# Kernel optimization log

Hardware: AMD Instinct MI355X
Metric: run time of the kernel (lower is better)

The kernel has to match this reference:

```python
import jax, jax.numpy as jnp
import numpy as np

NUM_HEADS = 8
LN_EPS = 1e-5


def setup_inputs() -> dict:
    key = jax.random.key(0)
    ks = jax.random.split(key, 8)
    B, H, W, C = 2, 64, 64, 256
    return {
        "x": jax.random.normal(ks[0], (B, H, W, C), dtype=jnp.float32),
        "cond": jax.random.normal(ks[1], (B, C), dtype=jnp.float32),
        "t": jax.random.randint(ks[2], (B,), 0, 100, dtype=jnp.int64),
        "emb_table": jax.random.normal(ks[3], (100, C), dtype=jnp.float32) * 0.02,
        "ada_w": jax.random.normal(ks[4], (C, 2 * C), dtype=jnp.float32) * 0.02,
        "ada_b": jnp.zeros((2 * C,), dtype=jnp.float32),
        "qkv_w": jax.random.normal(ks[5], (C, 3 * C), dtype=jnp.float32) * 0.02,
        "qkv_b": jnp.zeros((3 * C,), dtype=jnp.float32),
        "proj_w": jax.random.normal(ks[6], (C, C), dtype=jnp.float32) * 0.02,
        "proj_b": jnp.zeros((C,), dtype=jnp.float32),
    }


def reference(x, cond, t, emb_table, ada_w, ada_b, qkv_w, qkv_b, proj_w, proj_b):
    B, H, W, C = x.shape
    N = H * W
    h = NUM_HEADS
    d = C // h
    scale = d ** -0.5

    x = x.reshape(B, N, C)

    # AdaLayerNorm (adalayernorm_abs): timestep embedding -> SiLU -> Linear -> scale/shift
    emb = emb_table[t]                                # [B, C]
    ss = jax.nn.silu(emb) @ ada_w + ada_b             # [B, 2C]
    sc, sh = jnp.split(ss, 2, axis=-1)                # each [B, C]
    mu = jnp.mean(x, axis=-1, keepdims=True)
    var = jnp.var(x, axis=-1, keepdims=True)
    xn = (x - mu) * jax.lax.rsqrt(var + LN_EPS)       # LN without affine
    x = xn * (1.0 + sc[:, None, :]) + sh[:, None, :]

    # QKV projection and head split
    qkv = (x @ qkv_w + qkv_b).reshape(B, N, 3, h, d)
    qkv = jnp.transpose(qkv, (2, 0, 3, 1, 4))          # [3, B, h, N, d]
    q, k, v = qkv[0], qkv[1], qkv[2]

    # Manual attention: full [B, h, N, N] scores (matches original module)
    attn = jnp.einsum('bhnd,bhmd->bhnm', q, k) * scale
    attn = jax.nn.softmax(attn, axis=-1)
    out = jnp.einsum('bhnm,bhmd->bhnd', attn, v)       # [B, h, N, d]
    out = jnp.transpose(out, (0, 2, 1, 3)).reshape(B, N, C)

    out = (out.reshape(B, H, W, C) @ proj_w) + proj_b
    return out
```

## Files before the change

kernel.cpp:

```cpp
#include <hip/hip_runtime.h>
#include <hip/hip_bf16.h>
#include <stdint.h>

typedef __attribute__((ext_vector_type(8))) short bfrag;
typedef __attribute__((ext_vector_type(4))) short bfrag4;
typedef __attribute__((ext_vector_type(4))) float f32x4;
typedef __attribute__((ext_vector_type(2))) float f32x2;
typedef __attribute__((ext_vector_type(2))) unsigned int u32x2;

__device__ inline short f2bf(float f) {
  union { float f; uint32_t u; } v; v.f = f;
  uint32_t u = v.u;
  uint32_t r = (u + 0x7fffu + ((u >> 16) & 1u)) >> 16;
  return (short)r;
}
__device__ inline float bf2f(short s) {
  return __builtin_bit_cast(float, (uint32_t)((uint32_t)(uint16_t)s << 16));
}

#if __has_builtin(__builtin_amdgcn_cvt_pk_bf16_f32)
typedef __attribute__((ext_vector_type(2))) __bf16 bf16x2_t;
__device__ inline uint32_t pack_bf16(float a, float b) {
  bf16x2_t r = __builtin_amdgcn_cvt_pk_bf16_f32(a, b);
  return __builtin_bit_cast(uint32_t, r);
}
#else
__device__ inline uint32_t pack_bf16(float a, float b) {
  uint32_t ua = __builtin_bit_cast(uint32_t, a) + 0x8000u;
  uint32_t ub = __builtin_bit_cast(uint32_t, b) + 0x8000u;
  return __builtin_amdgcn_perm(ub, ua, 0x07060302);
}
#endif

__global__ __launch_bounds__(256) void prep_kernel(
    const float* __restrict__ emb_table, const int* __restrict__ t,
    const float* __restrict__ ada_w, const float* __restrict__ ada_b,
    float* __restrict__ scsh,
    const float* __restrict__ qkv_w, short* __restrict__ qkv_wt,
    const float* __restrict__ proj_w, short* __restrict__ proj_wt) {
  __shared__ float smem[64 * 65];
  const int blk = blockIdx.x;
  const int tid = threadIdx.x;
  if (blk < 16) {
    float* se = smem;
    float* part = smem + 256;
    int b = blk >> 3, ox = blk & 7;
    int tt = t[b];
    float e = emb_table[tt * 256 + tid];
    se[tid] = e / (1.f + __expf(-e));
    __syncthreads();
    int ol = tid & 63, kc = tid >> 6;
    int o = ox * 64 + ol;
    float acc = 0.f;
#pragma unroll 8
    for (int k = kc * 64; k < (kc + 1) * 64; ++k) acc += se[k] * ada_w[k * 512 + o];
    part[tid] = acc;
    __syncthreads();
    if (tid < 64) {
      int oo = ox * 64 + tid;
      scsh[b * 512 + oo] =
          part[tid] + part[64 + tid] + part[128 + tid] + part[192 + tid] + ada_b[oo];
    }
  } else {
    const float* W; short* Wt; int N, lb;
    if (blk < 64) { W = qkv_w; Wt = qkv_wt; N = 768; lb = blk - 16; }
    else          { W = proj_w; Wt = proj_wt; N = 256; lb = blk - 64; }
    float (*tile)[65] = (float(*)[65])smem;
    int k0 = (lb & 3) * 64, n0 = (lb >> 2) * 64;
    int r = tid >> 2, c0 = (tid & 3) * 16;
    const float* src = W + (long)(k0 + r) * N + n0 + c0;
#pragma unroll
    for (int j = 0; j < 16; j += 4) {
      float4 v = *(const float4*)(src + j);
      tile[r][c0 + j] = v.x; tile[r][c0 + j + 1] = v.y;
      tile[r][c0 + j + 2] = v.z; tile[r][c0 + j + 3] = v.w;
    }
    __syncthreads();
    int nl = tid >> 2, kc = (tid & 3) * 16;
    short outv[16];
#pragma unroll
    for (int j = 0; j < 16; ++j) outv[j] = f2bf(tile[kc + j][nl]);
    short* dst = Wt + (long)(n0 + nl) * 256 + k0 + kc;
    *(bfrag*)dst = *(bfrag*)&outv[0];
    *(bfrag*)(dst + 8) = *(bfrag*)&outv[8];
  }
}

__global__ __launch_bounds__(256) void ln_kernel(const float* __restrict__ x,
                                                 const float* __restrict__ scsh,
                                                 short* __restrict__ xb) {
  int row = blockIdx.x * 4 + (threadIdx.x >> 6);
  int b = row >> 12;
  int lane = threadIdx.x & 63;
  float4 v = *(const float4*)(x + (long)row * 256 + lane * 4);
  float s = v.x + v.y + v.z + v.w;
  float sq = v.x * v.x + v.y * v.y + v.z * v.z + v.w * v.w;
#pragma unroll
  for (int off = 32; off > 0; off >>= 1) {
    s += __shfl_xor(s, off);
    sq += __shfl_xor(sq, off);
  }
  float mu = s * (1.f / 256.f);
  float var = sq * (1.f / 256.f) - mu * mu;
  float rstd = rsqrtf(var + 1e-5f);
  const float* scp = scsh + b * 512 + lane * 4;
  float4 sc = *(const float4*)scp;
  float4 sh = *(const float4*)(scp + 256);
  float y0 = (v.x - mu) * rstd * (1.f + sc.x) + sh.x;
  float y1 = (v.y - mu) * rstd * (1.f + sc.y) + sh.y;
  float y2 = (v.z - mu) * rstd * (1.f + sc.z) + sh.z;
  float y3 = (v.w - mu) * rstd * (1.f + sc.w) + sh.w;
  u32x2 o; o.x = pack_bf16(y0, y1); o.y = pack_bf16(y2, y3);
  *(u32x2*)&xb[(long)row * 256 + lane * 4] = o;
}

__global__ __launch_bounds__(256) void gemm_bf16(const short* __restrict__ A,
                                                 const short* __restrict__ Bt,
                                                 const float* __restrict__ bias,
                                                 int N, int mode, float qscale,
                                                 short* __restrict__ qk,
                                                 short* __restrict__ vT,
                                                 float* __restrict__ cout) {
  __shared__ short As[128 * 40];
  __shared__ short Bs[64 * 40];
  const int mt = blockIdx.x, nt = blockIdx.y;
  const int tid = threadIdx.x;
  const int w = tid >> 6, lane = tid & 63, l16 = lane & 15, quad = lane >> 4;
  const int ar = tid >> 1, ak = (tid & 1) * 16;
  const int br = tid >> 2, bk = (tid & 3) * 8;
  f32x4 acc[2][4] = {};
  const short* Arow = A + (long)(mt * 128 + ar) * 256 + ak;
  const short* Brow = Bt + (long)(nt * 64 + br) * 256 + bk;
  bfrag a8a = *(const bfrag*)Arow;
  bfrag a8b = *(const bfrag*)(Arow + 8);
  bfrag b8  = *(const bfrag*)Brow;
  for (int kk = 0; kk < 8; ++kk) {
    __syncthreads();
    *(bfrag*)&As[ar * 40 + ak] = a8a;
    *(bfrag*)&As[ar * 40 + ak + 8] = a8b;
    *(bfrag*)&Bs[br * 40 + bk] = b8;
    __syncthreads();
    int kn = (kk < 7) ? (kk + 1) : 7;
    a8a = *(const bfrag*)(Arow + kn * 32);
    a8b = *(const bfrag*)(Arow + kn * 32 + 8);
    b8  = *(const bfrag*)(Brow + kn * 32);
    bfrag a0 = *(const bfrag*)&As[(w * 32 + l16) * 40 + quad * 8];
    bfrag a1 = *(const bfrag*)&As[(w * 32 + 16 + l16) * 40 + quad * 8];
#pragma unroll
    for (int c = 0; c < 4; ++c) {
      bfrag bf = *(const bfrag*)&Bs[(c * 16 + l16) * 40 + quad * 8];
      acc[0][c] = __builtin_amdgcn_mfma_f32_16x16x32_bf16(a0, bf, acc[0][c], 0, 0, 0);
      acc[1][c] = __builtin_amdgcn_mfma_f32_16x16x32_bf16(a1, bf, acc[1][c], 0, 0, 0);
    }
  }
  const int rowb = mt * 128 + w * 32 + quad * 4;
  if (mode == 1) {
#pragma unroll
    for (int rg = 0; rg < 2; ++rg) {
      int row0 = rowb + rg * 16;
#pragma unroll
      for (int c = 0; c < 4; ++c) {
        int col = nt * 64 + c * 16 + l16;
        float bv = bias[col];
#pragma unroll
        for (int r = 0; r < 4; ++r)
          cout[(long)(row0 + r) * N + col] = acc[rg][c][r] + bv;
      }
    }
  } else if (nt < 8) {
#pragma unroll
    for (int rg = 0; rg < 2; ++rg) {
      int row0 = rowb + rg * 16;
#pragma unroll
      for (int c = 0; c < 4; ++c) {
        int col = nt * 64 + c * 16 + l16;
        float bv = bias[col];
        float mult = (col < 256) ? qscale : 1.0f;
#pragma unroll
        for (int r = 0; r < 4; ++r)
          qk[(long)(row0 + r) * 512 + col] = f2bf((acc[rg][c][r] + bv) * mult);
      }
    }
  } else {
    const int bb = mt >> 5;
#pragma unroll
    for (int rg = 0; rg < 2; ++rg) {
      int keyl = (rowb + rg * 16) & 4095;
#pragma unroll
      for (int c = 0; c < 4; ++c) {
        int col = nt * 64 + c * 16 + l16;
        float bv = bias[col];
        int d = col - 512;
        u32x2 dd;
        dd.x = pack_bf16(acc[rg][c][0] + bv, acc[rg][c][1] + bv);
        dd.y = pack_bf16(acc[rg][c][2] + bv, acc[rg][c][3] + bv);
        *(u32x2*)&vT[((long)(bb * 8 + (d >> 5)) * 32 + (d & 31)) * 4096 + keyl] = dd;
      }
    }
  }
}

__global__ __launch_bounds__(256) void attn_kernel(const short* __restrict__ qk,
                                                   const short* __restrict__ vT,
                                                   short* __restrict__ OpB,
                                                   float* __restrict__ lpart) {
  const int blk = blockIdx.x;
  const int qt = blk & 15;
  const int bh = (blk >> 4) & 15;
  const int ks = blk >> 8;
  const int b = bh >> 3, hh = bh & 7;
  const int tid = threadIdx.x;
  const int w = tid >> 6, lane = tid & 63, l16 = lane & 15, quad = lane >> 4;

  __shared__ short Ks[2][64 * 40];
  __shared__ short Vt[2][32 * 68];

  const long rowbase = (long)b * 4096;
  const int qrow0 = qt * 256 + w * 64 + l16;
  bfrag qf[4];
#pragma unroll
  for (int g = 0; g < 4; ++g)
    qf[g] = *(const bfrag*)&qk[(rowbase + qrow0 + g * 16) * 512 + hh * 32 + quad * 8];

  f32x4 o0[4] = {}, o1[4] = {};
  f32x2 lsum[4] = {};

  const int si = tid >> 2, sk = (tid & 3) * 8;
  const int vrow = tid >> 3, vcol = (tid & 7) * 8;
  const short* ksrc = qk + rowbase * 512 + 256 + hh * 32 + (long)si * 512 + sk;
  const short* vsrc = vT + ((long)bh * 32 + vrow) * 4096 + vcol;

  const int kt0 = ks * 16;
  bfrag k8 = *(const bfrag*)(ksrc + (long)kt0 * 64 * 512);
  bfrag v8 = *(const bfrag*)(vsrc + kt0 * 64);

  int buf = 0;
  for (int i = 0; i < 16; ++i) {
    *(bfrag*)&Ks[buf][si * 40 + sk] = k8;
    *(bfrag*)&Vt[buf][vrow * 68 + vcol] = v8;
    __syncthreads();
    int nn = (i < 15) ? (i + 1) : 15;
    k8 = *(const bfrag*)(ksrc + (long)(kt0 + nn) * 64 * 512);
    v8 = *(const bfrag*)(vsrc + (kt0 + nn) * 64);

#pragma unroll
    for (int nt = 0; nt < 4; ++nt) {
      bfrag kf = *(const bfrag*)&Ks[buf][(nt * 16 + l16) * 40 + quad * 8];
      f32x4 z = {0,0,0,0};
      f32x4 s[4];
      s[0] = __builtin_amdgcn_mfma_f32_16x16x32_bf16(kf, qf[0], z, 0, 0, 0);
      s[1] = __builtin_amdgcn_mfma_f32_16x16x32_bf16(kf, qf[1], z, 0, 0, 0);
      s[2] = __builtin_amdgcn_mfma_f32_16x16x32_bf16(kf, qf[2], z, 0, 0, 0);
      s[3] = __builtin_amdgcn_mfma_f32_16x16x32_bf16(kf, qf[3], z, 0, 0, 0);
      bfrag4 pb[4];
#pragma unroll
      for (int g = 0; g < 4; ++g) {
        float p0 = __builtin_amdgcn_exp2f(s[g][0]);
        float p1 = __builtin_amdgcn_exp2f(s[g][1]);
        float p2 = __builtin_amdgcn_exp2f(s[g][2]);
        float p3 = __builtin_amdgcn_exp2f(s[g][3]);
        f32x2 pa = {p0, p1}, pc = {p2, p3};
        lsum[g] += pa; lsum[g] += pc;
        u32x2 pk; pk.x = pack_bf16(p0, p1); pk.y = pack_bf16(p2, p3);
        pb[g] = __builtin_bit_cast(bfrag4, pk);
      }
      bfrag4 va = *(const bfrag4*)&Vt[buf][l16 * 68 + nt * 16 + quad * 4];
      bfrag4 vb = *(const bfrag4*)&Vt[buf][(16 + l16) * 68 + nt * 16 + quad * 4];
#pragma unroll
      for (int g = 0; g < 4; ++g) {
        o0[g] = __builtin_amdgcn_mfma_f32_16x16x16bf16_1k(va, pb[g], o0[g], 0, 0, 0);
        o1[g] = __builtin_amdgcn_mfma_f32_16x16x16bf16_1k(vb, pb[g], o1[g], 0, 0, 0);
      }
    }
    buf ^= 1;
  }
#pragma unroll
  for (int g = 0; g < 4; ++g) {
    float ls = lsum[g].x + lsum[g].y;
    ls += __shfl_xor(ls, 16); ls += __shfl_xor(ls, 32);
    const long pbase = (((long)ks * 16 + bh) * 4096 + qrow0 + g * 16) * 32;
    u32x2 dA, dB;
    dA.x = pack_bf16(o0[g][0], o0[g][1]); dA.y = pack_bf16(o0[g][2], o0[g][3]);
    dB.x = pack_bf16(o1[g][0], o1[g][1]); dB.y = pack_bf16(o1[g][2], o1[g][3]);
    *(u32x2*)&OpB[pbase + quad * 4] = dA;
    *(u32x2*)&OpB[pbase + 16 + quad * 4] = dB;
    if (quad == 0)
      lpart[((long)ks * 16 + bh) * 4096 + qrow0 + g * 16] = ls;
  }
}

__global__ __launch_bounds__(256) void reduce_kernel(const short* __restrict__ OpB,
                                                     const float* __restrict__ lpart,
                                                     short* __restrict__ attn_out) {
  int row = blockIdx.x;
  int bq = row >> 12, q = row & 4095;
  int d = threadIdx.x;
  int h2 = d >> 5, dd = d & 31;
  int bh = bq * 8 + h2;
  float s = 0.f, l = 0.f;
#pragma unroll
  for (int ks = 0; ks < 4; ++ks) {
    long base = (long)(ks * 16 + bh) * 4096 + q;
    s += bf2f(OpB[base * 32 + dd]);
    l += lpart[base];
  }
  attn_out[(long)row * 256 + d] = f2bf(s / l);
}

extern "C" void kernel_launch(void* const* d_in, const int* in_sizes, int n_in,
                              void* d_out, int out_size, void* d_ws, size_t ws_size,
                              hipStream_t stream) {
  const float* x      = (const float*)d_in[0];
  const int*   t      = (const int*)d_in[2];
  const float* emb    = (const float*)d_in[3];
  const float* ada_w  = (const float*)d_in[4];
  const float* ada_b  = (const float*)d_in[5];
  const float* qkv_w  = (const float*)d_in[6];
  const float* qkv_b  = (const float*)d_in[7];
  const float* proj_w = (const float*)d_in[8];
  const float* proj_b = (const float*)d_in[9];

  char* ws = (char*)d_ws;
  float* scsh     = (float*)(ws);
  short* qkv_wt   = (short*)(ws + 4096);
  short* proj_wt  = (short*)(ws + 397312);
  short* xb       = (short*)(ws + 528384);
  short* qk_out   = (short*)(ws + 4722688);
  short* vT       = (short*)(ws + 13111296);
  short* attn_out = (short*)(ws + 17305600);
  short* OpB      = (short*)(ws + 21499904);
  float* lpart    = (float*)(ws + 38277120);

  const float QS = 0.17677669529663687f * 1.4426950408889634f;

  prep_kernel<<<80, 256, 0, stream>>>(emb, t, ada_w, ada_b, scsh,
                                      qkv_w, qkv_wt, proj_w, proj_wt);
  ln_kernel<<<2048, 256, 0, stream>>>(x, scsh, xb);
  gemm_bf16<<<dim3(64, 12), 256, 0, stream>>>(xb, qkv_wt, qkv_b, 768, 0, QS,
                                              qk_out, vT, nullptr);
  attn_kernel<<<1024, 256, 0, stream>>>(qk_out, vT, OpB, lpart);
  reduce_kernel<<<8192, 256, 0, stream>>>(OpB, lpart, attn_out);
  gemm_bf16<<<dim3(64, 4), 256, 0, stream>>>(attn_out, proj_wt, proj_b, 256, 1,
                                             1.0f, nullptr, nullptr, (float*)d_out);
}
```

Before: 169.7 us.

## Fuse split-KV partial reduction into the output projection GEMM A-loader

```diff
diff --git a/kernel.cpp b/kernel.cpp
--- a/kernel.cpp
+++ b/kernel.cpp
@@ -114,13 +114,12 @@
   *(u32x2*)&xb[(long)row * 256 + lane * 4] = o;
 }
 
-__global__ __launch_bounds__(256) void gemm_bf16(const short* __restrict__ A,
-                                                 const short* __restrict__ Bt,
-                                                 const float* __restrict__ bias,
-                                                 int N, int mode, float qscale,
-                                                 short* __restrict__ qk,
-                                                 short* __restrict__ vT,
-                                                 float* __restrict__ cout) {
+__global__ __launch_bounds__(256) void gemm_qkv(const short* __restrict__ A,
+                                                const short* __restrict__ Bt,
+                                                const float* __restrict__ bias,
+                                                float qscale,
+                                                short* __restrict__ qk,
+                                                short* __restrict__ vT) {
   __shared__ short As[128 * 40];
   __shared__ short Bs[64 * 40];
   const int mt = blockIdx.x, nt = blockIdx.y;
@@ -154,20 +153,7 @@
     }
   }
   const int rowb = mt * 128 + w * 32 + quad * 4;
-  if (mode == 1) {
-#pragma unroll
-    for (int rg = 0; rg < 2; ++rg) {
-      int row0 = rowb + rg * 16;
-#pragma unroll
-      for (int c = 0; c < 4; ++c) {
-        int col = nt * 64 + c * 16 + l16;
-        float bv = bias[col];
-#pragma unroll
-        for (int r = 0; r < 4; ++r)
-          cout[(long)(row0 + r) * N + col] = acc[rg][c][r] + bv;
-      }
-    }
-  } else if (nt < 8) {
+  if (nt < 8) {
 #pragma unroll
     for (int rg = 0; rg < 2; ++rg) {
       int row0 = rowb + rg * 16;
@@ -289,22 +275,88 @@
   }
 }
 
-__global__ __launch_bounds__(256) void reduce_kernel(const short* __restrict__ OpB,
-                                                     const float* __restrict__ lpart,
-                                                     short* __restrict__ attn_out) {
-  int row = blockIdx.x;
-  int bq = row >> 12, q = row & 4095;
-  int d = threadIdx.x;
-  int h2 = d >> 5, dd = d & 31;
-  int bh = bq * 8 + h2;
-  float s = 0.f, l = 0.f;
+__global__ __launch_bounds__(256) void proj_kernel(const short* __restrict__ OpB,
+                                                   const float* __restrict__ lpart,
+                                                   const short* __restrict__ Bt,
+                                                   const float* __restrict__ bias,
+                                                   float* __restrict__ out) {
+  __shared__ short As[128 * 40];
+  __shared__ short Bs[64 * 40];
+  const int mt = blockIdx.x, nt = blockIdx.y;
+  const int tid = threadIdx.x;
+  const int w = tid >> 6, lane = tid & 63, l16 = lane & 15, quad = lane >> 4;
+  const int ar = tid >> 1, ak = (tid & 1) * 16;
+  const int br = tid >> 2, bk = (tid & 3) * 8;
+  f32x4 acc[2][4] = {};
+
+  const int row = mt * 128 + ar;
+  const int q = row & 4095, bq = row >> 12;
+  const short* Brow = Bt + (long)(nt * 64 + br) * 256 + bk;
+
+  long lb0 = (long)(bq * 8) * 4096 + q;
+  bfrag pa[4][2];
+  f32x4 pl;
 #pragma unroll
   for (int ks = 0; ks < 4; ++ks) {
-    long base = (long)(ks * 16 + bh) * 4096 + q;
-    s += bf2f(OpB[base * 32 + dd]);
-    l += lpart[base];
-  }
-  attn_out[(long)row * 256 + d] = f2bf(s / l);
+    long base = (lb0 + (long)ks * 16 * 4096) * 32 + ak;
+    pa[ks][0] = *(const bfrag*)&OpB[base];
+    pa[ks][1] = *(const bfrag*)&OpB[base + 8];
+    pl[ks] = lpart[lb0 + (long)ks * 16 * 4096];
+  }
+  bfrag b8 = *(const bfrag*)Brow;
+
+  for (int kk = 0; kk < 8; ++kk) {
+    float linv = 1.f / (pl[0] + pl[1] + pl[2] + pl[3]);
+    short av[16];
+#pragma unroll
+    for (int h = 0; h < 2; ++h) {
+#pragma unroll
+      for (int j = 0; j < 8; j += 2) {
+        float v0 = (bf2f(pa[0][h][j]) + bf2f(pa[1][h][j]) +
+                    bf2f(pa[2][h][j]) + bf2f(pa[3][h][j])) * linv;
+        float v1 = (bf2f(pa[0][h][j+1]) + bf2f(pa[1][h][j+1]) +
+                    bf2f(pa[2][h][j+1]) + bf2f(pa[3][h][j+1])) * linv;
+        *(uint32_t*)&av[h * 8 + j] = pack_bf16(v0, v1);
+      }
+    }
+    __syncthreads();
+    *(bfrag*)&As[ar * 40 + ak] = *(bfrag*)&av[0];
+    *(bfrag*)&As[ar * 40 + ak + 8] = *(bfrag*)&av[8];
+    *(bfrag*)&Bs[br * 40 + bk] = b8;
+    __syncthreads();
+    int kn = (kk < 7) ? (kk + 1) : 7;
+    long lbn = (long)(bq * 8 + kn) * 4096 + q;
+#pragma unroll
+    for (int ks = 0; ks < 4; ++ks) {
+      long base = (lbn + (long)ks * 16 * 4096) * 32 + ak;
+      pa[ks][0] = *(const bfrag*)&OpB[base];
+      pa[ks][1] = *(const bfrag*)&OpB[base + 8];
+      pl[ks] = lpart[lbn + (long)ks * 16 * 4096];
+    }
+    b8 = *(const bfrag*)(Brow + kn * 32);
+
+    bfrag a0 = *(const bfrag*)&As[(w * 32 + l16) * 40 + quad * 8];
+    bfrag a1 = *(const bfrag*)&As[(w * 32 + 16 + l16) * 40 + quad * 8];
+#pragma unroll
+    for (int c = 0; c < 4; ++c) {
+      bfrag bf = *(const bfrag*)&Bs[(c * 16 + l16) * 40 + quad * 8];
+      acc[0][c] = __builtin_amdgcn_mfma_f32_16x16x32_bf16(a0, bf, acc[0][c], 0, 0, 0);
+      acc[1][c] = __builtin_amdgcn_mfma_f32_16x16x32_bf16(a1, bf, acc[1][c], 0, 0, 0);
+    }
+  }
+  const int rowb = mt * 128 + w * 32 + quad * 4;
+#pragma unroll
+  for (int rg = 0; rg < 2; ++rg) {
+    int row0 = rowb + rg * 16;
+#pragma unroll
+    for (int c = 0; c < 4; ++c) {
+      int col = nt * 64 + c * 16 + l16;
+      float bv = bias[col];
+#pragma unroll
+      for (int r = 0; r < 4; ++r)
+        out[(long)(row0 + r) * 256 + col] = acc[rg][c][r] + bv;
+    }
+  }
 }
 
 extern "C" void kernel_launch(void* const* d_in, const int* in_sizes, int n_in,
@@ -327,7 +379,6 @@
   short* xb       = (short*)(ws + 528384);
   short* qk_out   = (short*)(ws + 4722688);
   short* vT       = (short*)(ws + 13111296);
-  short* attn_out = (short*)(ws + 17305600);
   short* OpB      = (short*)(ws + 21499904);
   float* lpart    = (float*)(ws + 38277120);
 
@@ -336,10 +387,8 @@
   prep_kernel<<<80, 256, 0, stream>>>(emb, t, ada_w, ada_b, scsh,
                                       qkv_w, qkv_wt, proj_w, proj_wt);
   ln_kernel<<<2048, 256, 0, stream>>>(x, scsh, xb);
-  gemm_bf16<<<dim3(64, 12), 256, 0, stream>>>(xb, qkv_wt, qkv_b, 768, 0, QS,
-                                              qk_out, vT, nullptr);
+  gemm_qkv<<<dim3(64, 12), 256, 0, stream>>>(xb, qkv_wt, qkv_b, QS, qk_out, vT);
   attn_kernel<<<1024, 256, 0, stream>>>(qk_out, vT, OpB, lpart);
-  reduce_kernel<<<8192, 256, 0, stream>>>(OpB, lpart, attn_out);
-  gemm_bf16<<<dim3(64, 4), 256, 0, stream>>>(attn_out, proj_wt, proj_b, 256, 1,
-                                             1.0f, nullptr, nullptr, (float*)d_out);
-}
+  proj_kernel<<<dim3(64, 4), 256, 0, stream>>>(OpB, lpart, proj_wt, proj_b,
+                                               (float*)d_out);
+}
```

Result: no change. 166.7 us (-1.8%).
